# Kernel tuning notes

Measured on AMD Instinct MI355X. Metric: run time of the kernel, lower is better.

Reference implementation:

```python
import jax, jax.numpy as jnp
import numpy as np

EMBED_DIM = 1024
NUM_HEADS = 16
HEAD_DIM = EMBED_DIM // NUM_HEADS
ROPE_BASE = 10000.0


def _rope_angles(seq_len, head_dim):
    inv_freq = 1.0 / (ROPE_BASE ** (jnp.arange(0, head_dim, 2, dtype=jnp.float32) / head_dim))  # [D/2]
    pos = jnp.arange(seq_len, dtype=jnp.float32)
    ang = pos[:, None] * inv_freq[None, :]  # [S, D/2]
    return jnp.cos(ang), jnp.sin(ang)


def _apply_rope(t, cos, sin):
    # t: [B, H, S, D]; rotate-half convention
    d2 = t.shape[-1] // 2
    t1, t2 = t[..., :d2], t[..., d2:]
    return jnp.concatenate([t1 * cos - t2 * sin, t2 * cos + t1 * sin], axis=-1)


def setup_inputs() -> dict:
    key = jax.random.key(0)
    ks = jax.random.split(key, 6)
    B, S, E = 1, 4096, EMBED_DIM
    x = jax.random.normal(ks[0], (B, S, E), dtype=jnp.float32)
    # causal mask: True means masked-out (upper triangle above diagonal)
    mask = jnp.triu(jnp.ones((S, S), dtype=bool), k=1)[None, None, :, :]
    scale = 0.02
    wqkv_w = jax.random.normal(ks[1], (E, 3 * E), dtype=jnp.float32) * scale
    wqkv_b = jax.random.normal(ks[2], (3 * E,), dtype=jnp.float32) * scale
    out_w = jax.random.normal(ks[3], (E, E), dtype=jnp.float32) * scale
    out_b = jax.random.normal(ks[4], (E,), dtype=jnp.float32) * scale
    return {"x": x, "mask": mask, "wqkv_w": wqkv_w, "wqkv_b": wqkv_b, "out_w": out_w, "out_b": out_b}


def reference(x, mask, wqkv_w, wqkv_b, out_w, out_b):
    B, S, E = x.shape
    H, D = NUM_HEADS, HEAD_DIM
    qkv = x @ wqkv_w + wqkv_b  # [B, S, 3E]
    q, k, v = jnp.split(qkv, 3, axis=-1)
    # [B, S, E] -> [B, H, S, D]
    q = q.reshape(B, S, H, D).transpose(0, 2, 1, 3)
    k = k.reshape(B, S, H, D).transpose(0, 2, 1, 3)
    v = v.reshape(B, S, H, D).transpose(0, 2, 1, 3)
    cos, sin = _rope_angles(S, D)  # [S, D/2]
    q = _apply_rope(q, cos, sin)
    k = _apply_rope(k, cos, sin)
    scores = jnp.einsum('bhqd,bhkd->bhqk', q, k) * (D ** -0.5)  # [B, H, S, S]
    scores = jnp.where(mask[:, :, -S:, :], -jnp.inf, scores)
    weights = jax.nn.softmax(scores, axis=-1)
    ctx = jnp.einsum('bhqk,bhkd->bhqd', weights, v)  # [B, H, S, D]
    ctx = ctx.transpose(0, 2, 1, 3).reshape(B, S, E)
    return ctx @ out_w + out_b
```

## Files before the change

kernel.cpp:

```cpp
#include <hip/hip_runtime.h>
#include <hip/hip_bf16.h>
#include <math.h>

#define S_LEN 4096
#define EMB   1024
#define E3    3072
#define NH    16
#define HD    64

#define SLOTS_PER_HEAD 52
#define NSLOTS         832

typedef unsigned short u16;
typedef short          bfrag __attribute__((ext_vector_type(8)));
typedef float          ffrag __attribute__((ext_vector_type(4)));
typedef unsigned short us8   __attribute__((ext_vector_type(8)));
typedef unsigned short us4   __attribute__((ext_vector_type(4)));

__device__ __forceinline__ u16 f2bf(float f) {
    union { float f; unsigned u; } v; v.f = f;
    unsigned r = v.u + 0x7fffu + ((v.u >> 16) & 1u);
    return (u16)(r >> 16);
}
__device__ __forceinline__ float bf2f(u16 b) {
    union { unsigned u; float f; } v; v.u = ((unsigned)b) << 16;
    return v.f;
}
__device__ __forceinline__ unsigned pack_bf16_trunc(float lo, float hi) {
    union { float f; unsigned u; } a, b; a.f = lo; b.f = hi;
    return __builtin_amdgcn_perm(b.u, a.u, 0x07060302u);
}
__device__ __forceinline__ float fexp2(float x) {
    float r;
    asm("v_exp_f32 %0, %1" : "=v"(r) : "v"(x));
    return r;
}
__device__ __forceinline__ void pl32swap(unsigned &a, unsigned &b) {
    asm volatile("v_permlane32_swap_b32 %0, %1" : "+v"(a), "+v"(b));
}
__device__ __forceinline__ void pl16swap(unsigned &a, unsigned &b) {
    asm volatile("v_permlane16_swap_b32 %0, %1" : "+v"(a), "+v"(b));
}
__device__ __forceinline__ void gld16(const void* g, void* l) {
    __builtin_amdgcn_global_load_lds(
        (const __attribute__((address_space(1))) unsigned int*)g,
        (__attribute__((address_space(3))) unsigned int*)l, 16, 0, 0);
}

__device__ __forceinline__ void transpose_body(const float* __restrict__ in,
                                               u16* __restrict__ out,
                                               int R, int C, int bx, int by,
                                               u16 (*T)[72]) {
    const int r0 = bx * 64, c0 = by * 64;
    const int t = threadIdx.x;
    const int rr = t >> 2, cc = (t & 3) * 16;

    const float* ip = in + (size_t)(r0 + rr) * C + c0 + cc;
    u16 tmp[16];
    #pragma unroll
    for (int i4 = 0; i4 < 4; i4++) {
        float4 v = ((const float4*)ip)[i4];
        tmp[4*i4+0]=f2bf(v.x); tmp[4*i4+1]=f2bf(v.y);
        tmp[4*i4+2]=f2bf(v.z); tmp[4*i4+3]=f2bf(v.w);
    }
    #pragma unroll
    for (int i8 = 0; i8 < 2; i8++) {
        us8 vv;
        #pragma unroll
        for (int j = 0; j < 8; j++) vv[j] = tmp[8*i8+j];
        *(us8*)&T[rr][cc + 8*i8] = vv;
    }
    __syncthreads();

    const int oc = t >> 2, orr = (t & 3) * 16;
    u16 ot[16];
    #pragma unroll
    for (int j = 0; j < 16; j++) ot[j] = T[orr + j][oc];
    u16* op = out + (size_t)(c0 + oc) * R + r0 + orr;
    #pragma unroll
    for (int i8 = 0; i8 < 2; i8++) {
        us8 vv;
        #pragma unroll
        for (int j = 0; j < 8; j++) vv[j] = ot[8*i8+j];
        *(us8*)(op + 8*i8) = vv;
    }
}

__global__ __launch_bounds__(256)
void prep_kernel(const float* __restrict__ x, u16* __restrict__ xb,
                 const float* __restrict__ wqkv_w, u16* __restrict__ wt,
                 const float* __restrict__ out_w, u16* __restrict__ owt,
                 float2* __restrict__ tab) {
    __shared__ u16 T[64][72];
    const int b = blockIdx.x;
    if (b < 2048) {
        const size_t i = ((size_t)b * 256 + threadIdx.x) * 8;
        float4 a = *(const float4*)(x + i);
        float4 c = *(const float4*)(x + i + 4);
        us8 o;
        o[0]=f2bf(a.x); o[1]=f2bf(a.y); o[2]=f2bf(a.z); o[3]=f2bf(a.w);
        o[4]=f2bf(c.x); o[5]=f2bf(c.y); o[6]=f2bf(c.z); o[7]=f2bf(c.w);
        *(us8*)(xb + i) = o;
    } else if (b < 2816) {
        const int bb = b - 2048;
        transpose_body(wqkv_w, wt, EMB, E3, bb & 15, bb >> 4, T);
    } else if (b < 3072) {
        const int bb = b - 2816;
        transpose_body(out_w, owt, EMB, EMB, bb & 15, bb >> 4, T);
    } else {
        const int idx = (b - 3072) * 256 + threadIdx.x;
        const int s = idx >> 5, j = idx & 31;
        const float C = 13.287712379549449f / 32.0f;
        const float invf = exp2f(-(float)j * C);
        float sn, cs;
        sincosf((float)s * invf, &sn, &cs);
        tab[idx] = make_float2(cs, sn);
    }
}

template <int OUT_BF16, int NT, int ROPE, int MINW, int RBX, int RBY>
__global__ __launch_bounds__(256, MINW)
void gemm_bt_kernel(const u16* __restrict__ A, const u16* __restrict__ Bt,
                    const float* __restrict__ bias, void* __restrict__ Cv,
                    u16* __restrict__ vtp, const float2* __restrict__ rope,
                    int M, int N, int K) {
    constexpr int BN = 32 * NT;
    constexpr int WS = 16 * NT;
    __shared__ u16 As[2][128][32];
    __shared__ u16 Bs[2][BN][32];

    const int tid = threadIdx.x;
    const int w = tid >> 6, L = tid & 63;
    const int col = L & 15, quad = L >> 4;
    const int wm = w & 1, wn = w >> 1;

    const int bid = blockIdx.x + gridDim.x * blockIdx.y;
    const int xcd = bid & 7, ii = bid >> 3;
    const int bx = (xcd & 3) * RBX + (ii % RBX);
    const int by = (xcd >> 2) * RBY + (ii / RBX);
    const int m0 = bx * 128, n0 = by * BN;

    ffrag acc[4][NT];
    #pragma unroll
    for (int a = 0; a < 4; a++)
        #pragma unroll
        for (int b = 0; b < NT; b++)
            #pragma unroll
            for (int r = 0; r < 4; r++) acc[a][b][r] = 0.f;

    const int srow = L >> 2;
    const int schk = L & 3;

    #pragma unroll
    for (int t = 0; t < 2; t++) {
        const int rg = (2 * w + t) * 16;
        gld16(A + (size_t)(m0 + rg + srow) * K + schk * 8, &As[0][rg][0]);
    }
    #pragma unroll
    for (int t = 0; t < NT / 2; t++) {
        const int rg = (w * (NT / 2) + t) * 16;
        gld16(Bt + (size_t)(n0 + rg + srow) * K + schk * 8, &Bs[0][rg][0]);
    }
    __syncthreads();

    int buf = 0;
    for (int k0 = 0; k0 < K; k0 += 32, buf ^= 1) {
        if (k0 + 32 < K) {
            #pragma unroll
            for (int t = 0; t < 2; t++) {
                const int rg = (2 * w + t) * 16;
                gld16(A + (size_t)(m0 + rg + srow) * K + k0 + 32 + schk * 8,
                      &As[buf ^ 1][rg][0]);
            }
            #pragma unroll
            for (int t = 0; t < NT / 2; t++) {
                const int rg = (w * (NT / 2) + t) * 16;
                gld16(Bt + (size_t)(n0 + rg + srow) * K + k0 + 32 + schk * 8,
                      &Bs[buf ^ 1][rg][0]);
            }
        }

        bfrag af[4], bf[NT];
        #pragma unroll
        for (int mt = 0; mt < 4; mt++)
            af[mt] = *(const bfrag*)&As[buf][64 * wm + 16 * mt + col][8 * quad];
        #pragma unroll
        for (int nt = 0; nt < NT; nt++)
            bf[nt] = *(const bfrag*)&Bs[buf][WS * wn + 16 * nt + col][8 * quad];
        #pragma unroll
        for (int mt = 0; mt < 4; mt++)
            #pragma unroll
            for (int nt = 0; nt < NT; nt++)
                acc[mt][nt] = __builtin_amdgcn_mfma_f32_16x16x32_bf16(
                    af[mt], bf[nt], acc[mt][nt], 0, 0, 0);

        __syncthreads();
    }

    float bv[NT];
    #pragma unroll
    for (int nt = 0; nt < NT; nt++) bv[nt] = bias[n0 + WS * wn + 16 * nt + col];

    if (ROPE && n0 < 2 * EMB) {
        const float SCq = (n0 < EMB) ? 0.125f * 1.44269504088896f : 1.0f;
        #pragma unroll
        for (int mt = 0; mt < 4; mt++) {
            #pragma unroll
            for (int r = 0; r < 4; r++) {
                const int mrow = m0 + 64 * wm + 16 * mt + 4 * quad + r;
                u16* cp = (u16*)Cv + (size_t)mrow * N + n0 + 64 * wn + col;
                #pragma unroll
                for (int pr = 0; pr < 2; pr++) {
                    const float2 t = rope[(size_t)mrow * 32 + col + 16 * pr];
                    const float cs = t.x, sn = t.y;
                    const float t1 = acc[mt][pr][r] + bv[pr];
                    const float t2 = acc[mt][pr + 2][r] + bv[pr + 2];
                    cp[16 * pr]      = f2bf((t1 * cs - t2 * sn) * SCq);
                    cp[16 * pr + 32] = f2bf((t2 * cs + t1 * sn) * SCq);
                }
            }
        }
    } else if (ROPE) {
        #pragma unroll
        for (int nt = 0; nt < NT; nt++) {
            const int dg = n0 - 2 * EMB + WS * wn + 16 * nt + col;
            #pragma unroll
            for (int mt = 0; mt < 4; mt++) {
                const int s0 = m0 + 64 * wm + 16 * mt + 4 * quad;
                us4 pk;
                #pragma unroll
                for (int r = 0; r < 4; r++) pk[r] = f2bf(acc[mt][nt][r] + bv[nt]);
                *(us4*)&vtp[(size_t)dg * S_LEN + s0] = pk;
            }
        }
    } else {
        #pragma unroll
        for (int mt = 0; mt < 4; mt++) {
            #pragma unroll
            for (int r = 0; r < 4; r++) {
                const int m = m0 + 64 * wm + 16 * mt + 4 * quad + r;
                #pragma unroll
                for (int nt = 0; nt < NT; nt++) {
                    const int n = n0 + WS * wn + 16 * nt + col;
                    const float val = acc[mt][nt][r] + bv[nt];
                    if (OUT_BF16) ((u16*)Cv)[(size_t)m * N + n] = f2bf(val);
                    else          ((float*)Cv)[(size_t)m * N + n] = val;
                }
            }
        }
    }
}

__global__ __launch_bounds__(256, 4)
void flash16_kernel(const u16* __restrict__ qkvb, const u16* __restrict__ vt,
                    u16* __restrict__ ctxb, u16* __restrict__ pO,
                    float* __restrict__ pL) {
    __shared__ u16 QP[4][32][64];
    __shared__ u16 Ks[64][64];
    __shared__ u16 Vs[64][64];

    const int id = blockIdx.x;
    const int x  = id & 7;
    const int tt = id >> 3;
    const int h  = x + 8 * (tt & 1);
    const int o  = tt >> 1;

    int qi, ch, nc;
    if (o < 30)      { qi = 31 - o / 3;        ch = o % 3;        nc = 3; }
    else if (o < 33) { qi = 10 - (o - 30);     ch = 0;            nc = 1; }
    else if (o < 55) { const int oo = o - 33;  qi = 21 - oo / 2;  ch = oo & 1; nc = 2; }
    else             { qi = 7 - (o - 55);      ch = 0;            nc = 1; }

    const int total = 2 * qi + 2;
    const int Lc    = (total + nc - 1) / nc;
    const int kt0   = ch * Lc;
    const int cnt   = min(Lc, total - kt0);
    const bool lastch = (kt0 + cnt == total);
    const int q0 = qi * 128;

    const int tid = threadIdx.x;
    const int w = tid >> 6, L = tid & 63;
    const int col = L & 15, quad = L >> 4;
    const int lr = L >> 3, lp = L & 7;
    const int lc = lp ^ lr;

    const bool domask = lastch;
    const int nwt = cnt - ((domask && w < 2) ? 1 : 0);

    const size_t kArow = (size_t)(16 * w + lr) * E3 + EMB + h * HD + lc * 8;
    const size_t vArow = ((size_t)h * HD + 16 * w + lr) * S_LEN + lc * 8;
    const size_t kt0off  = (size_t)kt0 * 64 * E3;
    const size_t vt0off  = (size_t)kt0 * 64;

    #pragma unroll
    for (int u = 0; u < 4; u++)
        gld16(qkvb + (size_t)(q0 + 32 * w + 8 * u + lr) * E3 + h * HD + lc * 8,
              &QP[w][8 * u][0]);
    #pragma unroll
    for (int u = 0; u < 2; u++) {
        gld16(qkvb + kArow + kt0off + (size_t)(8 * u) * E3,
              &Ks[16 * w + 8 * u][0]);
        gld16(vt + vArow + vt0off + (size_t)(8 * u) * S_LEN,
              &Vs[16 * w + 8 * u][0]);
    }
    __syncthreads();

    bfrag qf[2][2];
    #pragma unroll
    for (int i = 0; i < 2; i++)
        #pragma unroll
        for (int ks = 0; ks < 2; ks++)
            qf[i][ks] = *(const bfrag*)
                ((const char*)&QP[w][16 * i + col][0] +
                 16 * ((4 * ks + quad) ^ (col & 7)));

    bfrag ones;
    #pragma unroll
    for (int i = 0; i < 8; i++) ones[i] = (short)0x3F80;
    const ffrag zf = {0.f, 0.f, 0.f, 0.f};

    ffrag o_[4][2], ol[2];
    #pragma unroll
    for (int d4 = 0; d4 < 4; d4++)
        #pragma unroll
        for (int i = 0; i < 2; i++)
            #pragma unroll
            for (int r2 = 0; r2 < 4; r2++) o_[d4][i][r2] = 0.f;
    #pragma unroll
    for (int i = 0; i < 2; i++)
        #pragma unroll
        for (int r2 = 0; r2 < 4; r2++) ol[i][r2] = 0.f;

    #pragma unroll 1
    for (int t = 0; t < cnt; t++) {
        bfrag pfr[2][2];
        if (t < nwt) {
            ffrag st[4][2];
            bfrag kf[4];
            #pragma unroll
            for (int t4 = 0; t4 < 4; t4++)
                kf[t4] = *(const bfrag*)
                    &Ks[16 * t4 + col][((quad ^ (col & 7)) * 8)];
            #pragma unroll
            for (int t4 = 0; t4 < 4; t4++)
                #pragma unroll
                for (int i = 0; i < 2; i++)
                    st[t4][i] = __builtin_amdgcn_mfma_f32_16x16x32_bf16(
                        kf[t4], qf[i][0], zf, 0, 0, 0);
            #pragma unroll
            for (int t4 = 0; t4 < 4; t4++)
                kf[t4] = *(const bfrag*)
                    &Ks[16 * t4 + col][(((4 + quad) ^ (col & 7)) * 8)];
            #pragma unroll
            for (int t4 = 0; t4 < 4; t4++)
                #pragma unroll
                for (int i = 0; i < 2; i++)
                    st[t4][i] = __builtin_amdgcn_mfma_f32_16x16x32_bf16(
                        kf[t4], qf[i][1], st[t4][i], 0, 0, 0);

            if (domask && t == nwt - 1) {
                #pragma unroll
                for (int i = 0; i < 2; i++) {
                    const int qrel = 32 * (w & 1) + 16 * i + col;
                    #pragma unroll
                    for (int t4 = 0; t4 < 4; t4++) {
                        const int key0 = 16 * t4 + 4 * quad;
                        #pragma unroll
                        for (int r2 = 0; r2 < 4; r2++)
                            if (key0 + r2 > qrel) st[t4][i][r2] = -3.0e38f;
                    }
                }
            }

            #pragma unroll
            for (int i = 0; i < 2; i++) {
                unsigned pku[4][2];
                #pragma unroll
                for (int t4 = 0; t4 < 4; t4++) {
                    float pr[4];
                    #pragma unroll
                    for (int r2 = 0; r2 < 4; r2++) pr[r2] = fexp2(st[t4][i][r2]);
                    pku[t4][0] = pack_bf16_trunc(pr[0], pr[1]);
                    pku[t4][1] = pack_bf16_trunc(pr[2], pr[3]);
                }
                #pragma unroll
                for (int ks = 0; ks < 2; ks++)
                    #pragma unroll
                    for (int hh = 0; hh < 2; hh++)
                        pl32swap(pku[2 * ks][hh], pku[2 * ks + 1][hh]);
                #pragma unroll
                for (int ks = 0; ks < 2; ks++)
                    #pragma unroll
                    for (int hh = 0; hh < 2; hh++)
                        pl16swap(pku[2 * ks][hh], pku[2 * ks + 1][hh]);
                #pragma unroll
                for (int ks = 0; ks < 2; ks++) {
                    union { unsigned u[4]; bfrag f; } ub;
                    ub.u[0] = pku[2 * ks][0];
                    ub.u[1] = pku[2 * ks][1];
                    ub.u[2] = pku[2 * ks + 1][0];
                    ub.u[3] = pku[2 * ks + 1][1];
                    pfr[i][ks] = ub.f;
                }
            }
        }

        __syncthreads();

        if (t + 1 < cnt) {
            const size_t ko = kArow + kt0off + (size_t)(t + 1) * 64 * E3;
            #pragma unroll
            for (int u = 0; u < 2; u++)
                gld16(qkvb + ko + (size_t)(8 * u) * E3, &Ks[16 * w + 8 * u][0]);
        }

        if (t < nwt) {
            #pragma unroll
            for (int ks = 0; ks < 2; ks++) {
                bfrag vf[4];
                #pragma unroll
                for (int d4 = 0; d4 < 4; d4++)
                    vf[d4] = *(const bfrag*)
                        &Vs[16 * d4 + col][(((4 * ks + quad) ^ (col & 7)) * 8)];
                #pragma unroll
                for (int d4 = 0; d4 < 4; d4++)
                    #pragma unroll
                    for (int i = 0; i < 2; i++)
                        o_[d4][i] = __builtin_amdgcn_mfma_f32_16x16x32_bf16(
                            vf[d4], pfr[i][ks], o_[d4][i], 0, 0, 0);
                #pragma unroll
                for (int i = 0; i < 2; i++)
                    ol[i] = __builtin_amdgcn_mfma_f32_16x16x32_bf16(
                        ones, pfr[i][ks], ol[i], 0, 0, 0);
            }
        }

        __syncthreads();

        if (t + 1 < cnt) {
            const size_t vo = vArow + vt0off + (size_t)(t + 1) * 64;
            #pragma unroll
            for (int u = 0; u < 2; u++)
                gld16(vt + vo + (size_t)(8 * u) * S_LEN, &Vs[16 * w + 8 * u][0]);
        }
    }

    if (nc == 1) {
        #pragma unroll
        for (int i = 0; i < 2; i++) {
            const float inv = 1.0f / ol[i][0];
            const int qg = q0 + 32 * w + 16 * i + col;
            #pragma unroll
            for (int d4 = 0; d4 < 4; d4++) {
                us4 pk;
                #pragma unroll
                for (int r2 = 0; r2 < 4; r2++) pk[r2] = f2bf(o_[d4][i][r2] * inv);
                *(us4*)&ctxb[(size_t)qg * EMB + h * HD + 16 * d4 + 4 * quad] = pk;
            }
        }
    } else {
        const int jj = (qi <= 21) ? (qi - 11) * 2 + ch : 22 + (qi - 22) * 3 + ch;
        const int slot = h * SLOTS_PER_HEAD + jj;
        u16* po = pO + (size_t)slot * (128 * 64);
        float* pl = pL + slot * 128;
        #pragma unroll
        for (int i = 0; i < 2; i++) {
            const int qrow = 32 * w + 16 * i + col;
            #pragma unroll
            for (int d4 = 0; d4 < 4; d4++) {
                us4 pk;
                #pragma unroll
                for (int r2 = 0; r2 < 4; r2++) pk[r2] = f2bf(o_[d4][i][r2]);
                *(us4*)&po[(size_t)qrow * 64 + 16 * d4 + 4 * quad] = pk;
            }
            if (quad == 0) pl[qrow] = ol[i][0];
        }
    }
}

__global__ __launch_bounds__(256)
void combine_kernel(const u16* __restrict__ pO, const float* __restrict__ pL,
                    u16* __restrict__ ctxb) {
    const int g = blockIdx.x;
    const int h = g / 21, qq = g % 21;
    const int qi = 11 + qq;
    const int nc = (qi <= 21) ? 2 : 3;
    const int jj0 = (qi <= 21) ? (qi - 11) * 2 : 22 + (qi - 22) * 3;
    const int slot0 = h * SLOTS_PER_HEAD + jj0;

    const int t = threadIdx.x;
    const int q = t >> 1, dh = (t & 1) * 32;

    float l = 0.f;
    for (int p = 0; p < nc; p++) l += pL[(slot0 + p) * 128 + q];
    const float inv = 1.0f / l;

    u16* op = ctxb + (size_t)(qi * 128 + q) * EMB + h * HD + dh;

    #pragma unroll
    for (int j = 0; j < 4; j++) {
        float s[8] = {0.f, 0.f, 0.f, 0.f, 0.f, 0.f, 0.f, 0.f};
        for (int p = 0; p < nc; p++) {
            const us8 va = *(const us8*)
                (pO + ((size_t)(slot0 + p) * 128 + q) * 64 + dh + 8 * j);
            #pragma unroll
            for (int e = 0; e < 8; e++) s[e] += bf2f(va[e]);
        }
        us8 vo;
        #pragma unroll
        for (int e = 0; e < 8; e++) vo[e] = f2bf(s[e] * inv);
        *(us8*)(op + 8 * j) = vo;
    }
}

extern "C" void kernel_launch(void* const* d_in, const int* in_sizes, int n_in,
                              void* d_out, int out_size, void* d_ws, size_t ws_size,
                              hipStream_t stream) {
    const float* x      = (const float*)d_in[0];
    const float* wqkv_w = (const float*)d_in[2];
    const float* wqkv_b = (const float*)d_in[3];
    const float* out_w  = (const float*)d_in[4];
    const float* out_b  = (const float*)d_in[5];
    float* out = (float*)d_out;

    u16* qkvb = (u16*)d_ws;
    u16* ctxb = qkvb + (size_t)S_LEN * E3;
    u16* xb   = ctxb + (size_t)S_LEN * EMB;
    u16* wt   = xb   + (size_t)S_LEN * EMB;
    u16* owt  = wt   + (size_t)E3 * EMB;
    u16* vtb  = owt  + (size_t)EMB * EMB;

    u16*   pO = xb;
    float* pL = (float*)(xb + (size_t)NSLOTS * 128 * 64);

    float2* ropetab = (float2*)ctxb;

    dim3 blk(256);

    prep_kernel<<<dim3(3584), blk, 0, stream>>>(
        x, xb, wqkv_w, wt, out_w, owt, ropetab);

    gemm_bt_kernel<1, 4, 1, 3, 8, 12>
        <<<dim3(S_LEN / 128, E3 / 128), blk, 0, stream>>>(
        xb, wt, wqkv_b, qkvb, vtb, ropetab, S_LEN, E3, EMB);

    flash16_kernel<<<dim3(1008), blk, 0, stream>>>(qkvb, vtb, ctxb, pO, pL);
    combine_kernel<<<dim3(336), blk, 0, stream>>>(pO, pL, ctxb);

    gemm_bt_kernel<0, 2, 0, 2, 8, 8>
        <<<dim3(S_LEN / 128, EMB / 64), blk, 0, stream>>>(
        ctxb, owt, out_b, out, nullptr, nullptr, S_LEN, EMB, EMB);
}
```

Baseline: 225.6 us.

## Double-buffer K/V tiles in flash kernel and load Q fragments directly

The flash attention kernel now keeps two shared-memory buffers each for K and V. At the start of each iteration it prefetches the next K/V tile into the idle buffer, which cuts the per-iteration barriers from two to one and lets global loads overlap the QK^T, softmax and PV MFMA work. The Q fragments are read straight from global memory into registers instead of being staged through a swizzled shared-memory tile. Total shared-memory use stays about the same. The risk is that uncoalesced direct Q loads and more outstanding loads per wave could add latency or register pressure.

```diff
diff --git a/kernel.cpp b/kernel.cpp
--- a/kernel.cpp
+++ b/kernel.cpp
@@ -252,12 +252,11 @@
 }
 
 __global__ __launch_bounds__(256, 4)
-void flash16_kernel(const u16* __restrict__ qkvb, const u16* __restrict__ vt,
+void flash17_kernel(const u16* __restrict__ qkvb, const u16* __restrict__ vt,
                     u16* __restrict__ ctxb, u16* __restrict__ pO,
                     float* __restrict__ pL) {
-    __shared__ u16 QP[4][32][64];
-    __shared__ u16 Ks[64][64];
-    __shared__ u16 Vs[64][64];
+    __shared__ u16 Ks[2][64][64];
+    __shared__ u16 Vs[2][64][64];
 
     const int id = blockIdx.x;
     const int x  = id & 7;
@@ -292,27 +291,23 @@
     const size_t kt0off  = (size_t)kt0 * 64 * E3;
     const size_t vt0off  = (size_t)kt0 * 64;
 
-    #pragma unroll
-    for (int u = 0; u < 4; u++)
-        gld16(qkvb + (size_t)(q0 + 32 * w + 8 * u + lr) * E3 + h * HD + lc * 8,
-              &QP[w][8 * u][0]);
+    bfrag qf[2][2];
+    #pragma unroll
+    for (int i = 0; i < 2; i++)
+        #pragma unroll
+        for (int ks = 0; ks < 2; ks++)
+            qf[i][ks] = *(const bfrag*)
+                (qkvb + (size_t)(q0 + 32 * w + 16 * i + col) * E3
+                      + h * HD + (4 * ks + quad) * 8);
+
     #pragma unroll
     for (int u = 0; u < 2; u++) {
         gld16(qkvb + kArow + kt0off + (size_t)(8 * u) * E3,
-              &Ks[16 * w + 8 * u][0]);
+              &Ks[0][16 * w + 8 * u][0]);
         gld16(vt + vArow + vt0off + (size_t)(8 * u) * S_LEN,
-              &Vs[16 * w + 8 * u][0]);
+              &Vs[0][16 * w + 8 * u][0]);
     }
     __syncthreads();
-
-    bfrag qf[2][2];
-    #pragma unroll
-    for (int i = 0; i < 2; i++)
-        #pragma unroll
-        for (int ks = 0; ks < 2; ks++)
-            qf[i][ks] = *(const bfrag*)
-                ((const char*)&QP[w][16 * i + col][0] +
-                 16 * ((4 * ks + quad) ^ (col & 7)));
 
     bfrag ones;
     #pragma unroll
@@ -333,14 +328,26 @@
 
     #pragma unroll 1
     for (int t = 0; t < cnt; t++) {
-        bfrag pfr[2][2];
+        const int buf = t & 1;
+        if (t + 1 < cnt) {
+            const size_t ko = kArow + kt0off + (size_t)(t + 1) * 64 * E3;
+            const size_t vo = vArow + vt0off + (size_t)(t + 1) * 64;
+            #pragma unroll
+            for (int u = 0; u < 2; u++) {
+                gld16(qkvb + ko + (size_t)(8 * u) * E3,
+                      &Ks[buf ^ 1][16 * w + 8 * u][0]);
+                gld16(vt + vo + (size_t)(8 * u) * S_LEN,
+                      &Vs[buf ^ 1][16 * w + 8 * u][0]);
+            }
+        }
+
         if (t < nwt) {
             ffrag st[4][2];
             bfrag kf[4];
             #pragma unroll
             for (int t4 = 0; t4 < 4; t4++)
                 kf[t4] = *(const bfrag*)
-                    &Ks[16 * t4 + col][((quad ^ (col & 7)) * 8)];
+                    &Ks[buf][16 * t4 + col][((quad ^ (col & 7)) * 8)];
             #pragma unroll
             for (int t4 = 0; t4 < 4; t4++)
                 #pragma unroll
@@ -350,7 +357,7 @@
             #pragma unroll
             for (int t4 = 0; t4 < 4; t4++)
                 kf[t4] = *(const bfrag*)
-                    &Ks[16 * t4 + col][(((4 + quad) ^ (col & 7)) * 8)];
+                    &Ks[buf][16 * t4 + col][(((4 + quad) ^ (col & 7)) * 8)];
             #pragma unroll
             for (int t4 = 0; t4 < 4; t4++)
                 #pragma unroll
@@ -372,6 +379,7 @@
                 }
             }
 
+            bfrag pfr[2][2];
             #pragma unroll
             for (int i = 0; i < 2; i++) {
                 unsigned pku[4][2];
@@ -403,25 +411,14 @@
                     pfr[i][ks] = ub.f;
                 }
             }
-        }
-
-        __syncthreads();
-
-        if (t + 1 < cnt) {
-            const size_t ko = kArow + kt0off + (size_t)(t + 1) * 64 * E3;
-            #pragma unroll
-            for (int u = 0; u < 2; u++)
-                gld16(qkvb + ko + (size_t)(8 * u) * E3, &Ks[16 * w + 8 * u][0]);
-        }
-
-        if (t < nwt) {
+
             #pragma unroll
             for (int ks = 0; ks < 2; ks++) {
                 bfrag vf[4];
                 #pragma unroll
                 for (int d4 = 0; d4 < 4; d4++)
                     vf[d4] = *(const bfrag*)
-                        &Vs[16 * d4 + col][(((4 * ks + quad) ^ (col & 7)) * 8)];
+                        &Vs[buf][16 * d4 + col][(((4 * ks + quad) ^ (col & 7)) * 8)];
                 #pragma unroll
                 for (int d4 = 0; d4 < 4; d4++)
                     #pragma unroll
@@ -436,13 +433,6 @@
         }
 
         __syncthreads();
-
-        if (t + 1 < cnt) {
-            const size_t vo = vArow + vt0off + (size_t)(t + 1) * 64;
-            #pragma unroll
-            for (int u = 0; u < 2; u++)
-                gld16(vt + vo + (size_t)(8 * u) * S_LEN, &Vs[16 * w + 8 * u][0]);
-        }
     }
 
     if (nc == 1) {
@@ -544,7 +534,7 @@
         <<<dim3(S_LEN / 128, E3 / 128), blk, 0, stream>>>(
         xb, wt, wqkv_b, qkvb, vtb, ropetab, S_LEN, E3, EMB);
 
-    flash16_kernel<<<dim3(1008), blk, 0, stream>>>(qkvb, vtb, ctxb, pO, pL);
+    flash17_kernel<<<dim3(1008), blk, 0, stream>>>(qkvb, vtb, ctxb, pO, pL);
     combine_kernel<<<dim3(336), blk, 0, stream>>>(pO, pL, ctxb);
 
     gemm_bt_kernel<0, 2, 0, 2, 8, 8>
```

Result: no change. 229.3 us, median of 2 (+1.7%).
